# Kernel optimization log

Hardware: AMD Instinct MI355X
Metric: run time of the kernel (lower is better)

Reference implementation:

```python
import jax, jax.numpy as jnp
import numpy as np

EMB = 1024
DM = 64
NH = 16

def setup_inputs() -> dict:
    key = jax.random.key(0)
    ks = jax.random.split(key, 11)
    bs, slen = 2, 2048
    s = 1.0 / np.sqrt(EMB)
    inp = {
        'Q': jax.random.normal(ks[0], (bs, slen, EMB), jnp.float32),
        'K': jax.random.normal(ks[1], (bs, slen, EMB), jnp.float32),
        'V': jax.random.normal(ks[2], (bs, slen, EMB), jnp.float32),
        'Wq': jax.random.normal(ks[3], (EMB, DM * NH), jnp.float32) * s,
        'bq': jnp.zeros((DM * NH,), jnp.float32),
        'Wk': jax.random.normal(ks[4], (EMB, DM * NH), jnp.float32) * s,
        'bk': jnp.zeros((DM * NH,), jnp.float32),
        'Wv': jax.random.normal(ks[5], (EMB, DM * NH), jnp.float32) * s,
        'bv': jnp.zeros((DM * NH,), jnp.float32),
        'Wo': jax.random.normal(ks[6], (DM * NH, EMB), jnp.float32) * (1.0 / np.sqrt(DM * NH)),
        'bo': jnp.zeros((EMB,), jnp.float32),
    }
    return inp

def reference(Q, K, V, Wq, bq, Wk, bk, Wv, bv, Wo, bo):
    bs, q_len, _ = Q.shape
    kv_len = K.shape[1]
    scale = 1.0 / np.sqrt(DM)
    # project and split heads: (n, l, h, d)
    q = (scale * (Q @ Wq + bq)).reshape(bs, q_len, NH, DM)
    k = (K @ Wk + bk).reshape(bs, kv_len, NH, DM)
    v = (V @ Wv + bv).reshape(bs, kv_len, NH, DM)
    # scores (n, h, l, s) -- full S x S matrix, as in the original
    qk = jnp.einsum('nlhd,nshd->nhls', q, k)
    a = jax.nn.softmax(qk, axis=-1)  # dropout p=0 -> identity
    o = jnp.einsum('nhls,nshd->nlhd', a, v).reshape(bs, q_len, NH * DM)
    return o @ Wo + bo
```

## Files before the change

### kernel.cpp

```cpp
#include <hip/hip_runtime.h>
#include <cstdint>
#include <cstddef>

#define EMB  1024
#define DM   64
#define NH   16
#define SLEN 2048
#define BS   2

typedef _Float16 f16x8 __attribute__((ext_vector_type(8)));
typedef _Float16 f16x4 __attribute__((ext_vector_type(4)));
typedef __fp16   hf2   __attribute__((ext_vector_type(2)));
typedef __fp16   hf4   __attribute__((ext_vector_type(4)));
typedef __fp16   hf8   __attribute__((ext_vector_type(8)));
typedef float    f32x4 __attribute__((ext_vector_type(4)));

#define ASYNC_LD16(gp, lp)                                                        \
    __builtin_amdgcn_global_load_lds(                                             \
        (const __attribute__((address_space(1))) void*)(gp),                      \
        (__attribute__((address_space(3))) void*)(lp), 16, 0, 0)

__global__ __launch_bounds__(256)
void prep(const float* __restrict__ Q, const float* __restrict__ K,
          const float* __restrict__ V,
          const float* __restrict__ Wq, const float* __restrict__ Wk,
          const float* __restrict__ Wv, const float* __restrict__ Wo,
          _Float16* __restrict__ Qh, _Float16* __restrict__ Kh,
          _Float16* __restrict__ Vh,
          _Float16* __restrict__ WqT, _Float16* __restrict__ WkT,
          _Float16* __restrict__ WvT, _Float16* __restrict__ WoT)
{
    __shared__ float t[64][65];
    const int z = blockIdx.z;
    if (z < 3) {
        const float* in  = (z == 0) ? Q : (z == 1) ? K : V;
        _Float16*    out = (z == 0) ? Qh : (z == 1) ? Kh : Vh;
        size_t i = ((size_t)blockIdx.x * 256 + threadIdx.x) * 8;
        float4 a = *(const float4*)(in + i);
        float4 b = *(const float4*)(in + i + 4);
        f16x8 o;
        o[0] = (_Float16)a.x; o[1] = (_Float16)a.y; o[2] = (_Float16)a.z; o[3] = (_Float16)a.w;
        o[4] = (_Float16)b.x; o[5] = (_Float16)b.y; o[6] = (_Float16)b.z; o[7] = (_Float16)b.w;
        *(f16x8*)(out + i) = o;
        return;
    }
    if (blockIdx.x >= 256) return;
    const float* W;
    _Float16*    T;
    switch (z - 3) {
        case 0:  W = Wq; T = WqT; break;
        case 1:  W = Wk; T = WkT; break;
        case 2:  W = Wv; T = WvT; break;
        default: W = Wo; T = WoT; break;
    }
    const int tid = threadIdx.x;
    const int bn  = (blockIdx.x & 15) * 64;
    const int bk  = (blockIdx.x >> 4) * 64;

    #pragma unroll
    for (int p = 0; p < 4; ++p) {
        int row = p * 16 + (tid >> 4);
        int col = (tid & 15) * 4;
        float4 v = *(const float4*)(W + (size_t)(bk + row) * EMB + bn + col);
        t[row][col+0] = v.x; t[row][col+1] = v.y; t[row][col+2] = v.z; t[row][col+3] = v.w;
    }
    __syncthreads();
    #pragma unroll
    for (int p = 0; p < 4; ++p) {
        int nr = p * 16 + (tid >> 4);
        int kc = (tid & 15) * 4;
        f16x4 o;
        o[0] = (_Float16)t[kc+0][nr];
        o[1] = (_Float16)t[kc+1][nr];
        o[2] = (_Float16)t[kc+2][nr];
        o[3] = (_Float16)t[kc+3][nr];
        *(f16x4*)&T[(size_t)(bn + nr) * EMB + bk + kc] = o;
    }
}

__device__ __forceinline__
void gemm_core(const _Float16* __restrict__ A, const _Float16* __restrict__ Bt,
               const float* __restrict__ bias, float* __restrict__ Cf,
               _Float16* __restrict__ Ch, int M, int N, int K,
               float scale, int mode, int bx, int by)
{
    __shared__ __align__(16) _Float16 As[128 * 32];
    __shared__ __align__(16) _Float16 Bs[128 * 32];

    const int tid  = threadIdx.x;
    const int lane = tid & 63;
    const int wave = tid >> 6;
    const int c    = lane & 15;
    const int quad = lane >> 4;
    const int bm   = by * 128;
    const int bn   = bx * 128;
    const int wm   = (wave >> 1) * 64;
    const int wn   = (wave & 1) * 64;

    f32x4 acc[4][4];
    #pragma unroll
    for (int i = 0; i < 4; ++i)
        #pragma unroll
        for (int j = 0; j < 4; ++j)
            #pragma unroll
            for (int r = 0; r < 4; ++r) acc[i][j][r] = 0.f;

    const char* gA = (const char*)(A + (size_t)(bm + (tid >> 2)) * K) + (tid & 3) * 16;
    const char* gB = (const char*)(Bt + (size_t)(bn + (tid >> 2)) * K) + (tid & 3) * 16;
    char* lA = (char*)As + wave * 1024;
    char* lB = (char*)Bs + wave * 1024;
    const size_t rowskip = (size_t)64 * K * 2;

    for (int k0 = 0; k0 < K; k0 += 32) {
        __syncthreads();
        ASYNC_LD16(gA + (size_t)k0 * 2,           lA);
        ASYNC_LD16(gA + rowskip + (size_t)k0 * 2, lA + 4096);
        ASYNC_LD16(gB + (size_t)k0 * 2,           lB);
        ASYNC_LD16(gB + rowskip + (size_t)k0 * 2, lB + 4096);
        __syncthreads();

        f16x8 af[4], bf[4];
        #pragma unroll
        for (int i = 0; i < 4; ++i)
            af[i] = *(const f16x8*)&As[(wm + i * 16 + c) * 32 + quad * 8];
        #pragma unroll
        for (int j = 0; j < 4; ++j)
            bf[j] = *(const f16x8*)&Bs[(wn + j * 16 + c) * 32 + quad * 8];

        #pragma unroll
        for (int i = 0; i < 4; ++i)
            #pragma unroll
            for (int j = 0; j < 4; ++j)
                acc[i][j] = __builtin_amdgcn_mfma_f32_16x16x32_f16(af[i], bf[j], acc[i][j], 0, 0, 0);
    }

    float bcol[4];
    #pragma unroll
    for (int j = 0; j < 4; ++j) bcol[j] = bias[bn + wn + j * 16 + c];

    #pragma unroll
    for (int i = 0; i < 4; ++i) {
        int m0 = bm + wm + i * 16 + quad * 4;
        #pragma unroll
        for (int j = 0; j < 4; ++j) {
            int n = bn + wn + j * 16 + c;
            if (mode == 0) {
                #pragma unroll
                for (int r = 0; r < 4; ++r)
                    Cf[(size_t)(m0 + r) * N + n] = acc[i][j][r] + bcol[j];
            } else if (mode == 1) {
                int h = n >> 6, d = n & 63;
                #pragma unroll
                for (int r = 0; r < 4; ++r) {
                    int mm = m0 + r;
                    int b = mm >> 11, l = mm & (SLEN - 1);
                    Ch[(((size_t)(b * NH + h)) * SLEN + l) * DM + d] =
                        (_Float16)((acc[i][j][r] + bcol[j]) * scale);
                }
            } else {
                int h = n >> 6, d = n & 63;
                int b = m0 >> 11, l = m0 & (SLEN - 1);
                f16x4 o;
                #pragma unroll
                for (int r = 0; r < 4; ++r)
                    o[r] = (_Float16)(acc[i][j][r] + bcol[j]);
                *(f16x4*)&Ch[(((size_t)(b * NH + h)) * DM + d) * SLEN + l] = o;
            }
        }
    }
}

__global__ __launch_bounds__(256)
void gemm_qkv(const _Float16* __restrict__ Qh, const _Float16* __restrict__ Kh,
              const _Float16* __restrict__ Vh,
              const _Float16* __restrict__ WqT, const _Float16* __restrict__ WkT,
              const _Float16* __restrict__ WvT,
              const float* __restrict__ bq, const float* __restrict__ bk,
              const float* __restrict__ bv,
              _Float16* __restrict__ q_ws, _Float16* __restrict__ k_ws,
              _Float16* __restrict__ v_ws)
{
    const _Float16 *A, *Bt;
    const float* bias;
    _Float16* Ch;
    float scale;
    int mode;
    if (blockIdx.z == 0)      { A = Qh; Bt = WqT; bias = bq; Ch = q_ws; scale = 0.18033688f; mode = 1; }
    else if (blockIdx.z == 1) { A = Kh; Bt = WkT; bias = bk; Ch = k_ws; scale = 1.0f;        mode = 1; }
    else                      { A = Vh; Bt = WvT; bias = bv; Ch = v_ws; scale = 1.0f;        mode = 2; }
    gemm_core(A, Bt, bias, nullptr, Ch, BS * SLEN, NH * DM, EMB, scale, mode,
              blockIdx.x, blockIdx.y);
}

__global__ __launch_bounds__(256)
void gemm_out(const _Float16* __restrict__ Oh, const _Float16* __restrict__ WoT,
              const float* __restrict__ bo, float* __restrict__ out)
{
    gemm_core(Oh, WoT, bo, out, nullptr, BS * SLEN, EMB, NH * DM, 1.0f, 0,
              blockIdx.x, blockIdx.y);
}

__global__ __launch_bounds__(512)
void attn_mfma(const _Float16* __restrict__ qw, const _Float16* __restrict__ kw,
               const _Float16* __restrict__ vwT, _Float16* __restrict__ ow)
{
    __shared__ __align__(16) _Float16 Kt[2][64 * 64];
    __shared__ __align__(16) _Float16 Vt[2][64 * 64];

    const int tid  = threadIdx.x;
    const int lane = tid & 63;
    const int wave = tid >> 6;
    const int c    = lane & 15;
    const int quad = lane >> 4;
    const int bh   = blockIdx.y;
    const int b    = bh >> 4;
    const int h    = bh & 15;
    const int qbase = blockIdx.x * 128 + wave * 16;

    const _Float16* kb = kw  + (size_t)bh * SLEN * DM;
    const _Float16* vb = vwT + (size_t)bh * DM * SLEN;
    const _Float16* qb = qw  + (size_t)bh * SLEN * DM;

    f16x8 qf[2];
    #pragma unroll
    for (int ch = 0; ch < 2; ++ch)
        qf[ch] = *(const f16x8*)(qb + (size_t)(qbase + c) * DM + ch*32 + quad*8);

    f32x4 oacc[4];
    f32x4 lacc;
    #pragma unroll
    for (int dg = 0; dg < 4; ++dg)
        #pragma unroll
        for (int r = 0; r < 4; ++r) oacc[dg][r] = 0.f;
    #pragma unroll
    for (int r = 0; r < 4; ++r) lacc[r] = 0.f;

    const f16x8 ones8 = {(_Float16)1.f, (_Float16)1.f, (_Float16)1.f, (_Float16)1.f,
                         (_Float16)1.f, (_Float16)1.f, (_Float16)1.f, (_Float16)1.f};
    const f32x4 zero4 = {0.f, 0.f, 0.f, 0.f};

    const int r0  = wave * 8 + (lane >> 3);
    const int lc0 = (((lane & 7) ^ ((lane >> 3) & 7)) * 16);
    const char* gk = (const char*)kb + r0 * 128 + lc0;
    const char* gv = (const char*)vb + (size_t)r0 * 4096 + lc0;
    char* lK = (char*)&Kt[0][0] + wave * 1024;
    char* lV = (char*)&Vt[0][0] + wave * 1024;

    ASYNC_LD16(gk, lK);
    ASYNC_LD16(gv, lV);
    gk += 8192; gv += 128;
    __syncthreads();

    auto tile = [&](int cur) {
        {
            char* pk = (char*)&Kt[cur ^ 1][0] + wave * 1024;
            char* pv = (char*)&Vt[cur ^ 1][0] + wave * 1024;
            ASYNC_LD16(gk, pk);
            ASYNC_LD16(gv, pv);
            gk += 8192; gv += 128;
        }

        f16x8 kf[4][2];
        #pragma unroll
        for (int g = 0; g < 4; ++g)
            #pragma unroll
            for (int ch = 0; ch < 2; ++ch)
                kf[g][ch] = *(const f16x8*)
                    &Kt[cur][(g*16 + c) * 64 + (((ch*4 + quad) ^ (c & 7)) * 8)];

        f32x4 s[4];
        #pragma unroll
        for (int g = 0; g < 4; ++g) {
            s[g] = __builtin_amdgcn_mfma_f32_16x16x32_f16(kf[g][0], qf[0], zero4, 0, 0, 0);
            s[g] = __builtin_amdgcn_mfma_f32_16x16x32_f16(kf[g][1], qf[1], s[g],  0, 0, 0);
        }

        f16x8 pf8[2];
        #pragma unroll
        for (int kk = 0; kk < 2; ++kk) {
            hf4 h4[2];
            #pragma unroll
            for (int u = 0; u < 2; ++u) {
                float p0 = __builtin_amdgcn_exp2f(s[2*kk + u][0]);
                float p1 = __builtin_amdgcn_exp2f(s[2*kk + u][1]);
                float p2 = __builtin_amdgcn_exp2f(s[2*kk + u][2]);
                float p3 = __builtin_amdgcn_exp2f(s[2*kk + u][3]);
                hf2 lo = __builtin_amdgcn_cvt_pkrtz(p0, p1);
                hf2 hi = __builtin_amdgcn_cvt_pkrtz(p2, p3);
                h4[u] = __builtin_shufflevector(lo, hi, 0, 1, 2, 3);
            }
            hf8 h8 = __builtin_shufflevector(h4[0], h4[1], 0, 1, 2, 3, 4, 5, 6, 7);
            pf8[kk] = __builtin_bit_cast(f16x8, h8);
        }

        #pragma unroll
        for (int kk = 0; kk < 2; ++kk)
            lacc = __builtin_amdgcn_mfma_f32_16x16x32_f16(pf8[kk], ones8, lacc, 0, 0, 0);

        #pragma unroll
        for (int dg = 0; dg < 4; ++dg) {
            f16x4 vf[4];
            #pragma unroll
            for (int g = 0; g < 4; ++g)
                vf[g] = *(const f16x4*)
                    &Vt[cur][(dg*16 + c) * 64 +
                             (((2*g + (quad >> 1)) ^ (c & 7)) * 8) + (quad & 1) * 4];
            f16x8 v01 = __builtin_shufflevector(vf[0], vf[1], 0, 1, 2, 3, 4, 5, 6, 7);
            f16x8 v23 = __builtin_shufflevector(vf[2], vf[3], 0, 1, 2, 3, 4, 5, 6, 7);
            oacc[dg] = __builtin_amdgcn_mfma_f32_16x16x32_f16(pf8[0], v01, oacc[dg], 0, 0, 0);
            oacc[dg] = __builtin_amdgcn_mfma_f32_16x16x32_f16(pf8[1], v23, oacc[dg], 0, 0, 0);
        }
        __syncthreads();
    };

    for (int it = 0; it < SLEN / 64; it += 2) {
        tile(0);
        tile(1);
    }

    #pragma unroll
    for (int r = 0; r < 4; ++r) {
        float linv = 1.0f / lacc[r];
        int row = qbase + quad*4 + r;
        #pragma unroll
        for (int dg = 0; dg < 4; ++dg)
            ow[((size_t)b * SLEN + row) * EMB + h * DM + dg*16 + c] =
                (_Float16)(oacc[dg][r] * linv);
    }
}

extern "C" void kernel_launch(void* const* d_in, const int* in_sizes, int n_in,
                              void* d_out, int out_size, void* d_ws, size_t ws_size,
                              hipStream_t stream)
{
    const float* Q  = (const float*)d_in[0];
    const float* K  = (const float*)d_in[1];
    const float* V  = (const float*)d_in[2];
    const float* Wq = (const float*)d_in[3];
    const float* bq = (const float*)d_in[4];
    const float* Wk = (const float*)d_in[5];
    const float* bk = (const float*)d_in[6];
    const float* Wv = (const float*)d_in[7];
    const float* bv = (const float*)d_in[8];
    const float* Wo = (const float*)d_in[9];
    const float* bo = (const float*)d_in[10];
    float* out = (float*)d_out;

    const size_t MN = (size_t)BS * SLEN * NH * DM;
    const size_t WW = (size_t)EMB * NH * DM;

    _Float16* base = (_Float16*)d_ws;
    _Float16* Qh   = base;
    _Float16* Kh   = Qh  + MN;
    _Float16* Vh   = Kh  + MN;
    _Float16* WqT  = Vh  + MN;
    _Float16* WkT  = WqT + WW;
    _Float16* WvT  = WkT + WW;
    _Float16* WoT  = WvT + WW;
    _Float16* q_ws = WoT + WW;
    _Float16* k_ws = q_ws + MN;
    _Float16* v_ws = k_ws + MN;
    _Float16* o_ws = v_ws + MN;

    dim3 blk(256);

    prep<<<dim3(2048, 1, 7), blk, 0, stream>>>(Q, K, V, Wq, Wk, Wv, Wo,
                                               Qh, Kh, Vh, WqT, WkT, WvT, WoT);

    gemm_qkv<<<dim3(8, 32, 3), blk, 0, stream>>>(Qh, Kh, Vh, WqT, WkT, WvT,
                                                 bq, bk, bv, q_ws, k_ws, v_ws);

    attn_mfma<<<dim3(SLEN / 128, BS * NH), dim3(512), 0, stream>>>(q_ws, k_ws, v_ws, o_ws);

    gemm_out<<<dim3(8, 32, 1), blk, 0, stream>>>(o_ws, WoT, bo, out);
}
```

Measured before the change: 232.3 us.

## Split attention KV tile across wave pairs, reuse K/V fragments over two query tiles

Each wave now handles 32 query rows (two 16-row tiles) and half of each 64-key tile, instead of 16 query rows and the full tile. K and V fragments read from LDS are reused across both query tiles, roughly halving LDS read traffic per MFMA. The two key-halves' partial outputs and row sums are combined through shared memory at the end, and the final iteration skips the out-of-range prefetch. This adds accumulator registers and an LDS reduction epilogue with extra barriers.

Result: faster. 224.8 us (-3.2%).

```diff
diff --git a/kernel.cpp b/kernel.cpp
--- a/kernel.cpp
+++ b/kernel.cpp
@@ -212,28 +212,35 @@
     const int wave = tid >> 6;
     const int c    = lane & 15;
     const int quad = lane >> 4;
+    const int qg   = wave & 3;
+    const int kh   = wave >> 2;
     const int bh   = blockIdx.y;
     const int b    = bh >> 4;
     const int h    = bh & 15;
-    const int qbase = blockIdx.x * 128 + wave * 16;
+    const int qbase = blockIdx.x * 128 + qg * 32;
 
     const _Float16* kb = kw  + (size_t)bh * SLEN * DM;
     const _Float16* vb = vwT + (size_t)bh * DM * SLEN;
     const _Float16* qb = qw  + (size_t)bh * SLEN * DM;
 
-    f16x8 qf[2];
-    #pragma unroll
-    for (int ch = 0; ch < 2; ++ch)
-        qf[ch] = *(const f16x8*)(qb + (size_t)(qbase + c) * DM + ch*32 + quad*8);
-
-    f32x4 oacc[4];
-    f32x4 lacc;
-    #pragma unroll
-    for (int dg = 0; dg < 4; ++dg)
-        #pragma unroll
-        for (int r = 0; r < 4; ++r) oacc[dg][r] = 0.f;
-    #pragma unroll
-    for (int r = 0; r < 4; ++r) lacc[r] = 0.f;
+    f16x8 qf[2][2];
+    #pragma unroll
+    for (int t = 0; t < 2; ++t)
+        #pragma unroll
+        for (int ch = 0; ch < 2; ++ch)
+            qf[t][ch] = *(const f16x8*)(qb + (size_t)(qbase + t*16 + c) * DM + ch*32 + quad*8);
+
+    f32x4 oacc[2][4];
+    f32x4 lacc[2];
+    #pragma unroll
+    for (int t = 0; t < 2; ++t) {
+        #pragma unroll
+        for (int dg = 0; dg < 4; ++dg)
+            #pragma unroll
+            for (int r = 0; r < 4; ++r) oacc[t][dg][r] = 0.f;
+        #pragma unroll
+        for (int r = 0; r < 4; ++r) lacc[t][r] = 0.f;
+    }
 
     const f16x8 ones8 = {(_Float16)1.f, (_Float16)1.f, (_Float16)1.f, (_Float16)1.f,
                          (_Float16)1.f, (_Float16)1.f, (_Float16)1.f, (_Float16)1.f};
@@ -251,8 +258,8 @@
     gk += 8192; gv += 128;
     __syncthreads();
 
-    auto tile = [&](int cur) {
-        {
+    auto tile = [&](int cur, bool pf) {
+        if (pf) {
             char* pk = (char*)&Kt[cur ^ 1][0] + wave * 1024;
             char* pv = (char*)&Vt[cur ^ 1][0] + wave * 1024;
             ASYNC_LD16(gk, pk);
@@ -260,72 +267,99 @@
             gk += 8192; gv += 128;
         }
 
-        f16x8 kf[4][2];
-        #pragma unroll
-        for (int g = 0; g < 4; ++g)
+        f16x8 kf[2][2];
+        #pragma unroll
+        for (int kg = 0; kg < 2; ++kg)
             #pragma unroll
             for (int ch = 0; ch < 2; ++ch)
-                kf[g][ch] = *(const f16x8*)
-                    &Kt[cur][(g*16 + c) * 64 + (((ch*4 + quad) ^ (c & 7)) * 8)];
-
-        f32x4 s[4];
-        #pragma unroll
-        for (int g = 0; g < 4; ++g) {
-            s[g] = __builtin_amdgcn_mfma_f32_16x16x32_f16(kf[g][0], qf[0], zero4, 0, 0, 0);
-            s[g] = __builtin_amdgcn_mfma_f32_16x16x32_f16(kf[g][1], qf[1], s[g],  0, 0, 0);
-        }
+                kf[kg][ch] = *(const f16x8*)
+                    &Kt[cur][(kh*32 + kg*16 + c) * 64 + (((ch*4 + quad) ^ (c & 7)) * 8)];
+
+        f32x4 s[2][2];
+        #pragma unroll
+        for (int t = 0; t < 2; ++t)
+            #pragma unroll
+            for (int kg = 0; kg < 2; ++kg) {
+                s[t][kg] = __builtin_amdgcn_mfma_f32_16x16x32_f16(kf[kg][0], qf[t][0], zero4,   0, 0, 0);
+                s[t][kg] = __builtin_amdgcn_mfma_f32_16x16x32_f16(kf[kg][1], qf[t][1], s[t][kg], 0, 0, 0);
+            }
 
         f16x8 pf8[2];
         #pragma unroll
-        for (int kk = 0; kk < 2; ++kk) {
+        for (int t = 0; t < 2; ++t) {
             hf4 h4[2];
             #pragma unroll
             for (int u = 0; u < 2; ++u) {
-                float p0 = __builtin_amdgcn_exp2f(s[2*kk + u][0]);
-                float p1 = __builtin_amdgcn_exp2f(s[2*kk + u][1]);
-                float p2 = __builtin_amdgcn_exp2f(s[2*kk + u][2]);
-                float p3 = __builtin_amdgcn_exp2f(s[2*kk + u][3]);
+                float p0 = __builtin_amdgcn_exp2f(s[t][u][0]);
+                float p1 = __builtin_amdgcn_exp2f(s[t][u][1]);
+                float p2 = __builtin_amdgcn_exp2f(s[t][u][2]);
+                float p3 = __builtin_amdgcn_exp2f(s[t][u][3]);
                 hf2 lo = __builtin_amdgcn_cvt_pkrtz(p0, p1);
                 hf2 hi = __builtin_amdgcn_cvt_pkrtz(p2, p3);
                 h4[u] = __builtin_shufflevector(lo, hi, 0, 1, 2, 3);
             }
             hf8 h8 = __builtin_shufflevector(h4[0], h4[1], 0, 1, 2, 3, 4, 5, 6, 7);
-            pf8[kk] = __builtin_bit_cast(f16x8, h8);
-        }
-
-        #pragma unroll
-        for (int kk = 0; kk < 2; ++kk)
-            lacc = __builtin_amdgcn_mfma_f32_16x16x32_f16(pf8[kk], ones8, lacc, 0, 0, 0);
+            pf8[t] = __builtin_bit_cast(f16x8, h8);
+        }
+
+        #pragma unroll
+        for (int t = 0; t < 2; ++t)
+            lacc[t] = __builtin_amdgcn_mfma_f32_16x16x32_f16(pf8[t], ones8, lacc[t], 0, 0, 0);
 
         #pragma unroll
         for (int dg = 0; dg < 4; ++dg) {
-            f16x4 vf[4];
-            #pragma unroll
-            for (int g = 0; g < 4; ++g)
-                vf[g] = *(const f16x4*)
+            f16x4 vf[2];
+            #pragma unroll
+            for (int u = 0; u < 2; ++u)
+                vf[u] = *(const f16x4*)
                     &Vt[cur][(dg*16 + c) * 64 +
-                             (((2*g + (quad >> 1)) ^ (c & 7)) * 8) + (quad & 1) * 4];
-            f16x8 v01 = __builtin_shufflevector(vf[0], vf[1], 0, 1, 2, 3, 4, 5, 6, 7);
-            f16x8 v23 = __builtin_shufflevector(vf[2], vf[3], 0, 1, 2, 3, 4, 5, 6, 7);
-            oacc[dg] = __builtin_amdgcn_mfma_f32_16x16x32_f16(pf8[0], v01, oacc[dg], 0, 0, 0);
-            oacc[dg] = __builtin_amdgcn_mfma_f32_16x16x32_f16(pf8[1], v23, oacc[dg], 0, 0, 0);
+                             (((kh*4 + 2*u + (quad >> 1)) ^ (c & 7)) * 8) + (quad & 1) * 4];
+            f16x8 v8 = __builtin_shufflevector(vf[0], vf[1], 0, 1, 2, 3, 4, 5, 6, 7);
+            #pragma unroll
+            for (int t = 0; t < 2; ++t)
+                oacc[t][dg] = __builtin_amdgcn_mfma_f32_16x16x32_f16(pf8[t], v8, oacc[t][dg], 0, 0, 0);
         }
         __syncthreads();
     };
 
-    for (int it = 0; it < SLEN / 64; it += 2) {
-        tile(0);
-        tile(1);
-    }
-
-    #pragma unroll
-    for (int r = 0; r < 4; ++r) {
-        float linv = 1.0f / lacc[r];
-        int row = qbase + quad*4 + r;
-        #pragma unroll
-        for (int dg = 0; dg < 4; ++dg)
-            ow[((size_t)b * SLEN + row) * EMB + h * DM + dg*16 + c] =
-                (_Float16)(oacc[dg][r] * linv);
+    for (int it = 0; it < SLEN / 64 - 2; it += 2) {
+        tile(0, true);
+        tile(1, true);
+    }
+    tile(0, true);
+    tile(1, false);
+
+    float* mb = (float*)&Kt[0][0];
+    #pragma unroll
+    for (int t = 0; t < 2; ++t) {
+        if (kh == 1) {
+            float* p = mb + ((qg * 64 + lane) * 20);
+            *(f32x4*)(p +  0) = oacc[t][0];
+            *(f32x4*)(p +  4) = oacc[t][1];
+            *(f32x4*)(p +  8) = oacc[t][2];
+            *(f32x4*)(p + 12) = oacc[t][3];
+            *(f32x4*)(p + 16) = lacc[t];
+        }
+        __syncthreads();
+        if (kh == 0) {
+            const float* p = mb + ((qg * 64 + lane) * 20);
+            f32x4 po[4], pl;
+            po[0] = *(const f32x4*)(p +  0);
+            po[1] = *(const f32x4*)(p +  4);
+            po[2] = *(const f32x4*)(p +  8);
+            po[3] = *(const f32x4*)(p + 12);
+            pl    = *(const f32x4*)(p + 16);
+            #pragma unroll
+            for (int r = 0; r < 4; ++r) {
+                float linv = 1.0f / (lacc[t][r] + pl[r]);
+                int row = qbase + t*16 + quad*4 + r;
+                #pragma unroll
+                for (int dg = 0; dg < 4; ++dg)
+                    ow[((size_t)b * SLEN + row) * EMB + h * DM + dg*16 + c] =
+                        (_Float16)((oacc[t][dg][r] + po[dg][r]) * linv);
+            }
+        }
+        __syncthreads();
     }
 }
 
```
